# Performance work log

Measured on AMD Instinct MI355X. Metric: run time of the kernel, lower is better.

Reference implementation:

```python
import jax, jax.numpy as jnp
import numpy as np

S, B, H = 1024, 4, 1024
NH, NC = 16, 4            # num_attention_heads, num_combined_heads
HPH = H // NH             # 64
NF = NH // NC             # num_FFN = 4
FFM = 8                   # combined_FFN_multiple
DIN = NC * HPH            # 256, grouped FFN input dim
DHID = FFM * DIN          # 2048, dense_in output dim
DH2 = DHID // 2           # 1024, GLU half / dense_out input dim
EPS = 1e-6
NORM_FACTOR = 1.0 / float(np.sqrt(HPH))


def _ln(x, g, b):
    m = x.mean(-1, keepdims=True)
    v = ((x - m) ** 2).mean(-1, keepdims=True)
    return (x - m) * jax.lax.rsqrt(v + EPS) * g + b


def setup_inputs() -> dict:
    key = jax.random.key(0)
    ks = jax.random.split(key, 10)
    p = lambda k, shape: jax.random.normal(k, shape, jnp.float32) * 0.02
    return {
        "hidden_states": jax.random.normal(ks[0], (S, B, H), jnp.float32),
        "g1": jnp.ones((H,), jnp.float32), "b1": jnp.zeros((H,), jnp.float32),
        "g2": jnp.ones((HPH,), jnp.float32), "b2": jnp.zeros((HPH,), jnp.float32),
        "Wq": p(ks[1], (H, H)), "bq": jnp.zeros((H,), jnp.float32),
        "Wk": p(ks[2], (H, H)), "bk": jnp.zeros((H,), jnp.float32),
        "Wv": p(ks[3], (H, H)), "bv": jnp.zeros((H,), jnp.float32),
        "W_in": p(ks[4], (NF, DIN, DHID)), "b_in": jnp.zeros((NF, DHID), jnp.float32),
        "W_out": p(ks[5], (NF, DH2, DIN)), "b_out": jnp.zeros((NF, DIN), jnp.float32),
        "Wd": p(ks[6], (H, H)), "bd": jnp.zeros((H,), jnp.float32),
    }


def reference(hidden_states, g1, b1, g2, b2, Wq, bq, Wk, bk, Wv, bv,
              W_in, b_in, W_out, b_out, Wd, bd):
    # hidden_states: [S, B, H]
    x = _ln(hidden_states, g1, b1)                       # norm1

    def heads(t):  # [S,B,H] -> [B*NH, S, HPH] (matches view + transpose in torch)
        return jnp.transpose(t.reshape(S, B * NH, HPH), (1, 0, 2))

    q = heads(x @ Wq + bq)
    k = heads(x @ Wk + bk)
    v = heads(x @ Wv + bv)

    # subtraction_gaussian_kernel: pairwise squared euclidean distance
    qk = jnp.einsum('nsd,ntd->nst', q, k)                # [B*NH, S, S]
    q2 = jnp.sum(q * q, axis=-1)
    k2 = jnp.sum(k * k, axis=-1)
    dist = q2[:, :, None] + k2[None if False else slice(None), None, :][0] if False else q2[:, :, None] + k2[:, None, :] - 2.0 * qk
    matmul_result = dist * (-0.5 * NORM_FACTOR)          # scores <= 0

    # Exp sequence op: elementwise exp (softmax replacement, no normalization)
    probs = jnp.exp(matmul_result)

    ctx = jnp.einsum('nst,ntd->nsd', probs, v)           # [B*NH, S, HPH]
    ctx = jnp.transpose(ctx, (1, 0, 2)).reshape(S, B, H)
    ctx = x + ctx                                        # residual with norm1 output (as in source)

    ctx = _ln(ctx.reshape(S, B, NH, HPH), g2, b2)        # per-head norm2

    # grouped FFN over contiguous head subsets (vectorized over the NF groups)
    cg = ctx.reshape(S, B, NF, DIN)
    h = jnp.einsum('sbgi,gio->sbgo', cg, W_in) + b_in    # [S,B,NF,DHID]
    xh, yh = jnp.split(h, 2, axis=-1)
    h = xh * jax.nn.relu(yh)                             # GLU-style x * relu(y)
    og = jnp.einsum('sbgi,gio->sbgo', h, W_out) + b_out  # [S,B,NF,DIN]

    out = og.reshape(S, B, H) @ Wd + bd                  # attention_dense
    return out, matmul_result
```

## Files before the change

kernel.cpp:

```cpp
#include <hip/hip_runtime.h>


typedef __attribute__((ext_vector_type(8))) short short8;
typedef __attribute__((ext_vector_type(4))) float f32x4;

__device__ __forceinline__ unsigned short f2bf(float f) {
  union { float f; unsigned u; } x; x.f = f;
  unsigned r = x.u + 0x7FFFu + ((x.u >> 16) & 1u);
  return (unsigned short)(r >> 16);
}
__device__ __forceinline__ float bf2f(unsigned short u) {
  union { float f; unsigned u; } x; x.u = ((unsigned)u) << 16;
  return x.f;
}
__device__ __forceinline__ unsigned cvtpk(float a, float b) {
  unsigned r;
  asm("v_cvt_pk_bf16_f32 %0, %1, %2" : "=v"(r) : "v"(a), "v"(b));
  return r;
}
__device__ __forceinline__ void gload16(const unsigned short* g, unsigned short* l) {
  __builtin_amdgcn_global_load_lds(
      (const __attribute__((address_space(1))) unsigned int*)g,
      (__attribute__((address_space(3))) unsigned int*)l, 16, 0, 0);
}

__device__ __forceinline__ void ln1_body(
    const float* __restrict__ x, const float* __restrict__ g,
    const float* __restrict__ b,
    unsigned short* __restrict__ ybf, int row, int tid)
{
  const long base = (long)row * 1024;
  const int c = tid * 4;
  float4 v = *(const float4*)(x + base + c);
  float s = v.x + v.y + v.z + v.w;
  float ss = v.x*v.x + v.y*v.y + v.z*v.z + v.w*v.w;
  #pragma unroll
  for (int off = 32; off > 0; off >>= 1) {
    s  += __shfl_xor(s, off);
    ss += __shfl_xor(ss, off);
  }
  __shared__ float sw[4], ssw[4];
  const int wave = tid >> 6;
  if ((tid & 63) == 0) { sw[wave] = s; ssw[wave] = ss; }
  __syncthreads();
  s  = sw[0] + sw[1] + sw[2] + sw[3];
  ss = ssw[0] + ssw[1] + ssw[2] + ssw[3];
  const float mean = s * (1.0f/1024.0f);
  const float var  = ss * (1.0f/1024.0f) - mean*mean;
  const float rs   = rsqrtf(var + 1e-6f);
  const float4 gv = *(const float4*)(g + c);
  const float4 bv = *(const float4*)(b + c);
  const float o0 = (v.x - mean) * rs * gv.x + bv.x;
  const float o1 = (v.y - mean) * rs * gv.y + bv.y;
  const float o2 = (v.z - mean) * rs * gv.z + bv.z;
  const float o3 = (v.w - mean) * rs * gv.w + bv.w;
  uint2 pk; pk.x = cvtpk(o0, o1); pk.y = cvtpk(o2, o3);
  *(uint2*)(ybf + base + c) = pk;
}

__device__ __forceinline__ void transpose_body(
    const float* __restrict__ Wg, unsigned short* __restrict__ WTg,
    int K, int N, int bx, int by, int tid)
{
  __shared__ float T[32][33];
  const int n0 = bx * 32, k0 = by * 32;
  const int r = tid >> 3, c4 = (tid & 7) * 4;
  float4 v = *(const float4*)(Wg + (long)(k0 + r) * N + n0 + c4);
  T[r][c4+0] = v.x; T[r][c4+1] = v.y; T[r][c4+2] = v.z; T[r][c4+3] = v.w;
  __syncthreads();
  ushort4 o;
  o.x = f2bf(T[c4+0][r]); o.y = f2bf(T[c4+1][r]);
  o.z = f2bf(T[c4+2][r]); o.w = f2bf(T[c4+3][r]);
  *(ushort4*)(WTg + (long)(n0 + r) * K + k0 + c4) = o;
}

__global__ __launch_bounds__(256) void prep_all_kernel(
    const float* __restrict__ hs, const float* __restrict__ g1,
    const float* __restrict__ b1,
    unsigned short* __restrict__ xbf,
    const float* __restrict__ Wq, const float* __restrict__ Wk,
    const float* __restrict__ Wv, const float* __restrict__ Wd,
    const float* __restrict__ Win, const float* __restrict__ Wout,
    const float* __restrict__ bq, const float* __restrict__ bk,
    const float* __restrict__ bv,
    unsigned short* __restrict__ wqkvT, unsigned short* __restrict__ wdT,
    unsigned short* __restrict__ winT, unsigned short* __restrict__ woutT,
    float* __restrict__ qkvb)
{
  const int bid = blockIdx.x;
  const int tid = threadIdx.x;
  if (bid < 4096) {
    ln1_body(hs, g1, b1, xbf, bid, tid);
  } else if (bid < 8192) {
    const int idx = bid - 4096;
    const int z = idx >> 10, rem = idx & 1023;
    const float* W = (z == 0) ? Wq : (z == 1) ? Wk : (z == 2) ? Wv : Wd;
    unsigned short* WT = (z == 3) ? wdT : wqkvT + (long)z * 1048576;
    transpose_body(W, WT, 1024, 1024, rem & 31, rem >> 5, tid);
  } else if (bid < 10240) {
    const int rem = bid - 8192;
    const int z = rem >> 9, r2 = rem & 511;
    transpose_body(Win + (long)z * 524288, winT + (long)z * 524288,
                   256, 2048, r2 & 63, r2 >> 6, tid);
  } else if (bid < 11264) {
    const int rem = bid - 10240;
    const int z = rem >> 8, r2 = rem & 255;
    transpose_body(Wout + (long)z * 262144, woutT + (long)z * 262144,
                   1024, 256, r2 & 7, r2 >> 3, tid);
  } else {
    const int i = (bid - 11264) * 256 + tid;
    qkvb[i] = (i < 1024) ? bq[i] : ((i < 2048) ? bk[i - 1024] : bv[i - 2048]);
  }
}

__global__ __launch_bounds__(256) void mfma_gemm_kernel(
    const unsigned short* __restrict__ A, int lda, long agoff,
    const unsigned short* __restrict__ BT, long bgoff, int K,
    const float* __restrict__ bias, int biasoff,
    unsigned short* __restrict__ Cbf, float* __restrict__ Cf,
    int ldc, int cgoff,
    float* __restrict__ q2g, float* __restrict__ k2g)
{
  const int g = blockIdx.z;
  const unsigned short* Ag = A + (long)g * agoff;
  const unsigned short* Bg = BT + (long)g * bgoff;
  const float* biasg = bias + (long)g * biasoff;
  const int row0 = blockIdx.y * 128, col0 = blockIdx.x * 128;
  __shared__ __align__(16) unsigned short As[2][128 * 64];
  __shared__ __align__(16) unsigned short Bs[2][128 * 64];
  const int tid = threadIdx.x;
  const int w = tid >> 6, l = tid & 63;
  const int ms = (w & 1) << 6, ns = (w >> 1) << 6;
  const int fr = l & 15, fg = l >> 4;
  const int lr8 = l >> 3, ls8 = l & 7;
  const int scol = (ls8 ^ lr8) << 3;
  const int rsw = fr & 7;
  f32x4 acc[4][4];
  #pragma unroll
  for (int i = 0; i < 4; ++i)
    #pragma unroll
    for (int j = 0; j < 4; ++j) acc[i][j] = (f32x4)0.0f;

  const int nt = K >> 6;
  #pragma unroll
  for (int sidx = 0; sidx < 2; ++sidx) {
    const int k0 = sidx << 6;
    #pragma unroll
    for (int g8 = 0; g8 < 4; ++g8) {
      const int r = (w << 5) + (g8 << 3);
      gload16(Ag + (long)(row0 + r + lr8) * lda + k0 + scol, &As[sidx][r * 64]);
      gload16(Bg + (long)(col0 + r + lr8) * K  + k0 + scol, &Bs[sidx][r * 64]);
    }
  }
  int cur = 0;
  for (int t = 0; t < nt; ++t) {
    if (t + 1 < nt) asm volatile("s_waitcnt vmcnt(8)" ::: "memory");
    else            asm volatile("s_waitcnt vmcnt(0)" ::: "memory");
    __builtin_amdgcn_s_barrier();
    __builtin_amdgcn_sched_barrier(0);
    short8 af[2][4], bfr[2][4];
    #pragma unroll
    for (int ks = 0; ks < 2; ++ks) {
      const int rslot = (((ks << 2) + fg) ^ rsw) << 3;
      #pragma unroll
      for (int i = 0; i < 4; ++i) {
        af[ks][i]  = *(const short8*)&As[cur][(ms + i*16 + fr) * 64 + rslot];
        bfr[ks][i] = *(const short8*)&Bs[cur][(ns + i*16 + fr) * 64 + rslot];
      }
    }
    asm volatile("s_waitcnt lgkmcnt(0)" ::: "memory");
    __builtin_amdgcn_sched_barrier(0);
    __builtin_amdgcn_s_barrier();
    if (t + 2 < nt) {
      const int k0 = (t + 2) << 6;
      #pragma unroll
      for (int g8 = 0; g8 < 4; ++g8) {
        const int r = (w << 5) + (g8 << 3);
        gload16(Ag + (long)(row0 + r + lr8) * lda + k0 + scol, &As[cur][r * 64]);
        gload16(Bg + (long)(col0 + r + lr8) * K  + k0 + scol, &Bs[cur][r * 64]);
      }
    }
    __builtin_amdgcn_s_setprio(1);
    #pragma unroll
    for (int ks = 0; ks < 2; ++ks)
      #pragma unroll
      for (int i = 0; i < 4; ++i)
        #pragma unroll
        for (int j = 0; j < 4; ++j)
          acc[i][j] = __builtin_amdgcn_mfma_f32_16x16x32_bf16(bfr[ks][j], af[ks][i], acc[i][j], 0, 0, 0);
    __builtin_amdgcn_s_setprio(0);
    cur ^= 1;
  }

  float s2[4] = {0.f, 0.f, 0.f, 0.f};
  #pragma unroll
  for (int j = 0; j < 4; ++j) {
    const float4 bj4 = *(const float4*)(biasg + col0 + ns + j*16 + (fg << 2));
    #pragma unroll
    for (int i = 0; i < 4; ++i) {
      const long row = row0 + ms + i*16 + fr;
      const long cb = row * ldc + (long)g * cgoff + col0 + ns + j*16 + (fg << 2);
      const float v0 = acc[i][j][0] + bj4.x, v1 = acc[i][j][1] + bj4.y;
      const float v2 = acc[i][j][2] + bj4.z, v3 = acc[i][j][3] + bj4.w;
      s2[i] += v0*v0 + v1*v1 + v2*v2 + v3*v3;
      if (Cbf) {
        uint2 pk; pk.x = cvtpk(v0, v1); pk.y = cvtpk(v2, v3);
        *(uint2*)(Cbf + cb) = pk;
      } else {
        f32x4 o = {v0, v1, v2, v3};
        __builtin_nontemporal_store(o, (f32x4*)(Cf + cb));
      }
    }
  }
  if (q2g && col0 < 2048) {
    const int nsAbs = col0 + ns;
    const bool isQ = nsAbs < 1024;
    float* outp = isQ ? q2g : k2g;
    const int head = (isQ ? nsAbs : nsAbs - 1024) >> 6;
    #pragma unroll
    for (int i = 0; i < 4; ++i) {
      float s = s2[i];
      s += __shfl_xor(s, 16);
      s += __shfl_xor(s, 32);
      if (fg == 0) {
        const int gr = row0 + ms + i*16 + fr;
        outp[((gr & 3) * 16 + head) * 1024 + (gr >> 2)] = s;
      }
    }
  }
}

__global__ __launch_bounds__(256) void mfma_gemm64_kernel(
    const unsigned short* __restrict__ A, int lda, long agoff,
    const unsigned short* __restrict__ BT, long bgoff, int K,
    const float* __restrict__ bias, int biasoff,
    unsigned short* __restrict__ Cbf, float* __restrict__ Cf,
    int ldc, int cgoff)
{
  const int g = blockIdx.z;
  const unsigned short* Ag = A + (long)g * agoff;
  const unsigned short* Bg = BT + (long)g * bgoff;
  const float* biasg = bias + (long)g * biasoff;
  const int row0 = blockIdx.y * 128, col0 = blockIdx.x * 64;
  __shared__ __align__(16) unsigned short As[2][128 * 64];
  __shared__ __align__(16) unsigned short Bs[2][64 * 64];
  const int tid = threadIdx.x;
  const int w = tid >> 6, l = tid & 63;
  const int ms = (w & 1) << 6, ns = (w >> 1) << 5;
  const int fr = l & 15, fg = l >> 4;
  const int lr8 = l >> 3, ls8 = l & 7;
  const int scol = (ls8 ^ lr8) << 3;
  const int rsw = fr & 7;
  f32x4 acc[4][2];
  #pragma unroll
  for (int i = 0; i < 4; ++i)
    #pragma unroll
    for (int j = 0; j < 2; ++j) acc[i][j] = (f32x4)0.0f;

  const int nt = K >> 6;
  #pragma unroll
  for (int sidx = 0; sidx < 2; ++sidx) {
    const int k0 = sidx << 6;
    #pragma unroll
    for (int g8 = 0; g8 < 4; ++g8) {
      const int r = (w << 5) + (g8 << 3);
      gload16(Ag + (long)(row0 + r + lr8) * lda + k0 + scol, &As[sidx][r * 64]);
    }
    #pragma unroll
    for (int g8 = 0; g8 < 2; ++g8) {
      const int r = (w << 4) + (g8 << 3);
      gload16(Bg + (long)(col0 + r + lr8) * K + k0 + scol, &Bs[sidx][r * 64]);
    }
  }
  int cur = 0;
  for (int t = 0; t < nt; ++t) {
    if (t + 1 < nt) asm volatile("s_waitcnt vmcnt(6)" ::: "memory");
    else            asm volatile("s_waitcnt vmcnt(0)" ::: "memory");
    __builtin_amdgcn_s_barrier();
    __builtin_amdgcn_sched_barrier(0);
    short8 af[2][4], bfr[2][2];
    #pragma unroll
    for (int ks = 0; ks < 2; ++ks) {
      const int rslot = (((ks << 2) + fg) ^ rsw) << 3;
      #pragma unroll
      for (int i = 0; i < 4; ++i)
        af[ks][i] = *(const short8*)&As[cur][(ms + i*16 + fr) * 64 + rslot];
      #pragma unroll
      for (int j = 0; j < 2; ++j)
        bfr[ks][j] = *(const short8*)&Bs[cur][(ns + j*16 + fr) * 64 + rslot];
    }
    asm volatile("s_waitcnt lgkmcnt(0)" ::: "memory");
    __builtin_amdgcn_sched_barrier(0);
    __builtin_amdgcn_s_barrier();
    if (t + 2 < nt) {
      const int k0 = (t + 2) << 6;
      #pragma unroll
      for (int g8 = 0; g8 < 4; ++g8) {
        const int r = (w << 5) + (g8 << 3);
        gload16(Ag + (long)(row0 + r + lr8) * lda + k0 + scol, &As[cur][r * 64]);
      }
      #pragma unroll
      for (int g8 = 0; g8 < 2; ++g8) {
        const int r = (w << 4) + (g8 << 3);
        gload16(Bg + (long)(col0 + r + lr8) * K + k0 + scol, &Bs[cur][r * 64]);
      }
    }
    __builtin_amdgcn_s_setprio(1);
    #pragma unroll
    for (int ks = 0; ks < 2; ++ks)
      #pragma unroll
      for (int i = 0; i < 4; ++i)
        #pragma unroll
        for (int j = 0; j < 2; ++j)
          acc[i][j] = __builtin_amdgcn_mfma_f32_16x16x32_bf16(bfr[ks][j], af[ks][i], acc[i][j], 0, 0, 0);
    __builtin_amdgcn_s_setprio(0);
    cur ^= 1;
  }

  #pragma unroll
  for (int j = 0; j < 2; ++j) {
    const float4 bj4 = *(const float4*)(biasg + col0 + ns + j*16 + (fg << 2));
    #pragma unroll
    for (int i = 0; i < 4; ++i) {
      const long row = row0 + ms + i*16 + fr;
      const long cb = row * ldc + (long)g * cgoff + col0 + ns + j*16 + (fg << 2);
      const float v0 = acc[i][j][0] + bj4.x, v1 = acc[i][j][1] + bj4.y;
      const float v2 = acc[i][j][2] + bj4.z, v3 = acc[i][j][3] + bj4.w;
      if (Cbf) {
        uint2 pk; pk.x = cvtpk(v0, v1); pk.y = cvtpk(v2, v3);
        *(uint2*)(Cbf + cb) = pk;
      } else {
        f32x4 o = {v0, v1, v2, v3};
        __builtin_nontemporal_store(o, (f32x4*)(Cf + cb));
      }
    }
  }
}

__global__ __launch_bounds__(256) void mfma_glu_kernel(
    const unsigned short* __restrict__ A,
    const unsigned short* __restrict__ WT,
    const float* __restrict__ bin,
    unsigned short* __restrict__ H2)
{
  const int g = blockIdx.z;
  const unsigned short* Ag = A + g * 256;
  const unsigned short* Wg = WT + (long)g * 2048 * 256;
  const float* bg = bin + g * 2048;
  const int row0 = blockIdx.y * 128, col0 = blockIdx.x * 64;
  __shared__ __align__(16) unsigned short As[2][128 * 64];
  __shared__ __align__(16) unsigned short Bxs[2][64 * 64];
  __shared__ __align__(16) unsigned short Bys[2][64 * 64];
  const int tid = threadIdx.x;
  const int w = tid >> 6, l = tid & 63;
  const int ms = (w & 1) << 6, ns = (w >> 1) << 5;
  const int fr = l & 15, fg = l >> 4;
  const int lr8 = l >> 3, ls8 = l & 7;
  const int scol = (ls8 ^ lr8) << 3;
  const int rsw = fr & 7;
  f32x4 ax[4][2], ay[4][2];
  #pragma unroll
  for (int i = 0; i < 4; ++i)
    #pragma unroll
    for (int j = 0; j < 2; ++j) { ax[i][j] = (f32x4)0.0f; ay[i][j] = (f32x4)0.0f; }

  #pragma unroll
  for (int sidx = 0; sidx < 2; ++sidx) {
    const int k0 = sidx << 6;
    #pragma unroll
    for (int g8 = 0; g8 < 4; ++g8) {
      const int r = (w << 5) + (g8 << 3);
      gload16(Ag + (long)(row0 + r + lr8) * 1024 + k0 + scol, &As[sidx][r * 64]);
    }
    #pragma unroll
    for (int g8 = 0; g8 < 2; ++g8) {
      const int r = (w << 4) + (g8 << 3);
      gload16(Wg + (long)(col0 + r + lr8) * 256 + k0 + scol,        &Bxs[sidx][r * 64]);
      gload16(Wg + (long)(1024 + col0 + r + lr8) * 256 + k0 + scol, &Bys[sidx][r * 64]);
    }
  }
  int cur = 0;
  for (int t = 0; t < 4; ++t) {
    if (t + 1 < 4) asm volatile("s_waitcnt vmcnt(8)" ::: "memory");
    else           asm volatile("s_waitcnt vmcnt(0)" ::: "memory");
    __builtin_amdgcn_s_barrier();
    __builtin_amdgcn_sched_barrier(0);
    short8 af[2][4], bx[2][2], by[2][2];
    #pragma unroll
    for (int ks = 0; ks < 2; ++ks) {
      const int rslot = (((ks << 2) + fg) ^ rsw) << 3;
      #pragma unroll
      for (int i = 0; i < 4; ++i)
        af[ks][i] = *(const short8*)&As[cur][(ms + i*16 + fr) * 64 + rslot];
      #pragma unroll
      for (int j = 0; j < 2; ++j) {
        bx[ks][j] = *(const short8*)&Bxs[cur][(ns + j*16 + fr) * 64 + rslot];
        by[ks][j] = *(const short8*)&Bys[cur][(ns + j*16 + fr) * 64 + rslot];
      }
    }
    asm volatile("s_waitcnt lgkmcnt(0)" ::: "memory");
    __builtin_amdgcn_sched_barrier(0);
    __builtin_amdgcn_s_barrier();
    if (t + 2 < 4) {
      const int k0 = (t + 2) << 6;
      #pragma unroll
      for (int g8 = 0; g8 < 4; ++g8) {
        const int r = (w << 5) + (g8 << 3);
        gload16(Ag + (long)(row0 + r + lr8) * 1024 + k0 + scol, &As[cur][r * 64]);
      }
      #pragma unroll
      for (int g8 = 0; g8 < 2; ++g8) {
        const int r = (w << 4) + (g8 << 3);
        gload16(Wg + (long)(col0 + r + lr8) * 256 + k0 + scol,        &Bxs[cur][r * 64]);
        gload16(Wg + (long)(1024 + col0 + r + lr8) * 256 + k0 + scol, &Bys[cur][r * 64]);
      }
    }
    __builtin_amdgcn_s_setprio(1);
    #pragma unroll
    for (int ks = 0; ks < 2; ++ks)
      #pragma unroll
      for (int i = 0; i < 4; ++i)
        #pragma unroll
        for (int j = 0; j < 2; ++j) {
          ax[i][j] = __builtin_amdgcn_mfma_f32_16x16x32_bf16(bx[ks][j], af[ks][i], ax[i][j], 0, 0, 0);
          ay[i][j] = __builtin_amdgcn_mfma_f32_16x16x32_bf16(by[ks][j], af[ks][i], ay[i][j], 0, 0, 0);
        }
    __builtin_amdgcn_s_setprio(0);
    cur ^= 1;
  }

  #pragma unroll
  for (int j = 0; j < 2; ++j) {
    const float4 bx4 = *(const float4*)(bg + col0 + ns + j*16 + (fg << 2));
    const float4 by4 = *(const float4*)(bg + 1024 + col0 + ns + j*16 + (fg << 2));
    #pragma unroll
    for (int i = 0; i < 4; ++i) {
      const long row = row0 + ms + i*16 + fr;
      const long cb = row * 4096 + g * 1024 + col0 + ns + j*16 + (fg << 2);
      float o4[4];
      const float* bxp = &bx4.x; const float* byp = &by4.x;
      #pragma unroll
      for (int r4 = 0; r4 < 4; ++r4) {
        const float xh = ax[i][j][r4] + bxp[r4];
        const float yh = ay[i][j][r4] + byp[r4];
        o4[r4] = xh * fmaxf(yh, 0.0f);
      }
      uint2 pk; pk.x = cvtpk(o4[0], o4[1]); pk.y = cvtpk(o4[2], o4[3]);
      *(uint2*)(H2 + cb) = pk;
    }
  }
}

__global__ __launch_bounds__(256) void vtrans_kernel(
    const unsigned short* __restrict__ qkv, unsigned short* __restrict__ vt)
{
  __shared__ unsigned short T[64][72];
  const int n = blockIdx.y, s0 = blockIdx.x * 64;
  const int b = n >> 4, hoff = (n & 15) * 64;
  const int tid = threadIdx.x;
  #pragma unroll
  for (int p = 0; p < 2; ++p) {
    const int r = (tid >> 3) + p * 32, c = (tid & 7) << 3;
    *(short8*)&T[r][c] = *(const short8*)(qkv + ((long)((s0 + r) * 4 + b)) * 3072 + 2048 + hoff + c);
  }
  __syncthreads();
  #pragma unroll
  for (int p = 0; p < 2; ++p) {
    const int d = (tid >> 3) + p * 32, sc = (tid & 7) << 3;
    short8 o;
    #pragma unroll
    for (int j = 0; j < 8; ++j) o[j] = (short)T[sc + j][d];
    *(short8*)(vt + ((long)n * 64 + d) * 1024 + s0 + sc) = o;
  }
}

__global__ __launch_bounds__(256) void attn_kernel(
    const unsigned short* __restrict__ qkv, const unsigned short* __restrict__ vt,
    const float* __restrict__ q2g, const float* __restrict__ k2g,
    const unsigned short* __restrict__ xbf, const float* __restrict__ g2,
    const float* __restrict__ b2,
    unsigned short* __restrict__ ctx2, float* __restrict__ scores)
{
  const int n = blockIdx.y;
  const int s0 = blockIdx.x * 64;
  const int b = n >> 4, hoff = (n & 15) * 64;
  __shared__ __align__(16) unsigned short Qs[64 * 64];
  __shared__ __align__(16) unsigned short Ks[2][64 * 64];
  __shared__ __align__(16) unsigned short VTl[2][64 * 64];
  __shared__ __align__(16) unsigned short Ps[64 * 64];
  __shared__ float k2s[1024];
  const int tid = threadIdx.x, w = tid >> 6, l = tid & 63;
  const int fr = l & 15, fg = l >> 4;
  const int lr8 = l >> 3, ls8 = l & 7;
  const int sslot = ((ls8 ^ lr8) << 3);
  const int rsw = fr & 7;

  #pragma unroll
  for (int p = 0; p < 2; ++p) {
    const int r = (tid >> 3) + p * 32, cs = tid & 7;
    *(short8*)&Qs[r * 64 + ((cs ^ (r & 7)) << 3)] =
        *(const short8*)(qkv + ((long)((s0 + r) * 4 + b)) * 3072 + hoff + (cs << 3));
  }
  *(float4*)&k2s[tid << 2] = *(const float4*)(k2g + n * 1024 + (tid << 2));
  float q2m[4];
  #pragma unroll
  for (int i = 0; i < 4; ++i) q2m[i] = -0.0625f * q2g[n * 1024 + s0 + i*16 + fr];
  #pragma unroll
  for (int p = 0; p < 2; ++p) {
    const int rowb = p * 32 + w * 8;
    gload16(qkv + ((long)((rowb + lr8) * 4 + b)) * 3072 + 1024 + hoff + sslot, &Ks[0][rowb * 64]);
    gload16(vt + ((long)n * 64 + rowb + lr8) * 1024 + sslot,                   &VTl[0][rowb * 64]);
  }
  __syncthreads();

  f32x4 o[4];
  #pragma unroll
  for (int i = 0; i < 4; ++i) o[i] = (f32x4)0.0f;

  int cur = 0;
  for (int t0 = 0; t0 < 1024; t0 += 64) {
    if (t0 > 0) {
      asm volatile("s_waitcnt vmcnt(4)" ::: "memory");
      __builtin_amdgcn_sched_barrier(0);
      __builtin_amdgcn_s_barrier();
    }
    f32x4 c4[4];
    #pragma unroll
    for (int i = 0; i < 4; ++i) c4[i] = (f32x4)0.0f;
    #pragma unroll
    for (int ks = 0; ks < 2; ++ks) {
      const short8 kf = *(const short8*)&Ks[cur][((w << 4) + fr) * 64 + ((((ks << 2) + fg) ^ rsw) << 3)];
      #pragma unroll
      for (int i = 0; i < 4; ++i) {
        const short8 qf = *(const short8*)&Qs[(i*16 + fr) * 64 + ((((ks << 2) + fg) ^ rsw) << 3)];
        c4[i] = __builtin_amdgcn_mfma_f32_16x16x32_bf16(kf, qf, c4[i], 0, 0, 0);
      }
    }
    if (t0 + 64 < 1024) {
      #pragma unroll
      for (int p = 0; p < 2; ++p) {
        const int rowb = p * 32 + w * 8;
        gload16(qkv + ((long)((t0 + 64 + rowb + lr8) * 4 + b)) * 3072 + 1024 + hoff + sslot,
                &Ks[cur ^ 1][rowb * 64]);
        gload16(vt + ((long)n * 64 + rowb + lr8) * 1024 + t0 + 64 + sslot,
                &VTl[cur ^ 1][rowb * 64]);
      }
    }
    const float4 k2v4 = *(const float4*)&k2s[t0 + (w << 4) + (fg << 2)];
    const float k2m[4] = {-0.0625f*k2v4.x, -0.0625f*k2v4.y, -0.0625f*k2v4.z, -0.0625f*k2v4.w};
    #pragma unroll
    for (int i = 0; i < 4; ++i) {
      f32x4 sc;
      float pe[4];
      #pragma unroll
      for (int r4 = 0; r4 < 4; ++r4) {
        const float m = fmaf(c4[i][r4], 0.125f, q2m[i] + k2m[r4]);
        sc[r4] = m;
        pe[r4] = __expf(m);
      }
      __builtin_nontemporal_store(sc,
          (f32x4*)(scores + (long)n * 1048576 + (long)(s0 + i*16 + fr) * 1024 + t0 + (w << 4) + (fg << 2)));
      const int slot = (w << 1) + (fg >> 1);
      const int pc = ((slot ^ (fr & 7)) << 3) + ((fg & 1) << 2);
      uint2 pk; pk.x = cvtpk(pe[0], pe[1]); pk.y = cvtpk(pe[2], pe[3]);
      *(uint2*)&Ps[(i*16 + fr) * 64 + pc] = pk;
    }
    asm volatile("s_waitcnt lgkmcnt(0)" ::: "memory");
    __builtin_amdgcn_sched_barrier(0);
    __builtin_amdgcn_s_barrier();
    #pragma unroll
    for (int ks = 0; ks < 2; ++ks) {
      const short8 vb = *(const short8*)&VTl[cur][((w << 4) + fr) * 64 + ((((ks << 2) + fg) ^ rsw) << 3)];
      #pragma unroll
      for (int i = 0; i < 4; ++i) {
        const short8 pf = *(const short8*)&Ps[(i*16 + fr) * 64 + ((((ks << 2) + fg) ^ rsw) << 3)];
        o[i] = __builtin_amdgcn_mfma_f32_16x16x32_bf16(vb, pf, o[i], 0, 0, 0);
      }
    }
    asm volatile("s_waitcnt lgkmcnt(0)" ::: "memory");
    __builtin_amdgcn_sched_barrier(0);
    __builtin_amdgcn_s_barrier();
    cur ^= 1;
  }

  const int dbase = (w << 4) + (fg << 2);
  float xf[4][4];
  #pragma unroll
  for (int i = 0; i < 4; ++i) {
    const ushort4 xu = *(const ushort4*)(xbf + ((long)((s0 + i*16 + fr) * 4 + b)) * 1024 + hoff + dbase);
    xf[i][0] = bf2f(xu.x); xf[i][1] = bf2f(xu.y);
    xf[i][2] = bf2f(xu.z); xf[i][3] = bf2f(xu.w);
  }

  float* redbuf = (float*)&Ps[0];
  const int slot = (w << 2) + fg;
  #pragma unroll
  for (int i = 0; i < 4; ++i) {
    float s = 0.f, ss = 0.f;
    #pragma unroll
    for (int r4 = 0; r4 < 4; ++r4) {
      const float v = o[i][r4] + xf[i][r4];
      s += v; ss = fmaf(v, v, ss);
    }
    redbuf[(i*16 + fr) * 16 + slot] = s;
    redbuf[1024 + (i*16 + fr) * 16 + slot] = ss;
  }
  __syncthreads();
  float* statbuf = (float*)&Qs[0];
  {
    const int row = tid >> 2, q4 = tid & 3;
    float s = 0.f, ss = 0.f;
    #pragma unroll
    for (int k = 0; k < 4; ++k) {
      s  += redbuf[row * 16 + q4 * 4 + k];
      ss += redbuf[1024 + row * 16 + q4 * 4 + k];
    }
    s  += __shfl_xor(s, 1);  s  += __shfl_xor(s, 2);
    ss += __shfl_xor(ss, 1); ss += __shfl_xor(ss, 2);
    if (q4 == 0) {
      const float mean = s * (1.0f/64.0f);
      const float var  = ss * (1.0f/64.0f) - mean * mean;
      statbuf[row] = mean;
      statbuf[64 + row] = rsqrtf(var + 1e-6f);
    }
  }
  __syncthreads();
  const float4 g2v = *(const float4*)(g2 + dbase);
  const float4 b2v = *(const float4*)(b2 + dbase);
  const float* gp = &g2v.x; const float* bp = &b2v.x;
  #pragma unroll
  for (int i = 0; i < 4; ++i) {
    const float mean = statbuf[i*16 + fr];
    const float rs   = statbuf[64 + i*16 + fr];
    float vo[4];
    #pragma unroll
    for (int r4 = 0; r4 < 4; ++r4)
      vo[r4] = (o[i][r4] + xf[i][r4] - mean) * rs * gp[r4] + bp[r4];
    uint2 pk; pk.x = cvtpk(vo[0], vo[1]); pk.y = cvtpk(vo[2], vo[3]);
    *(uint2*)(ctx2 + ((long)((s0 + i*16 + fr) * 4 + b)) * 1024 + hoff + dbase) = pk;
  }
}

extern "C" void kernel_launch(void* const* d_in, const int* in_sizes, int n_in,
                              void* d_out, int out_size, void* d_ws, size_t ws_size,
                              hipStream_t stream) {
  const float* hs   = (const float*)d_in[0];
  const float* g1   = (const float*)d_in[1];
  const float* b1   = (const float*)d_in[2];
  const float* g2   = (const float*)d_in[3];
  const float* b2   = (const float*)d_in[4];
  const float* Wq   = (const float*)d_in[5];
  const float* bq   = (const float*)d_in[6];
  const float* Wk   = (const float*)d_in[7];
  const float* bk   = (const float*)d_in[8];
  const float* Wv   = (const float*)d_in[9];
  const float* bv   = (const float*)d_in[10];
  const float* Win  = (const float*)d_in[11];
  const float* bin  = (const float*)d_in[12];
  const float* Wout = (const float*)d_in[13];
  const float* bout = (const float*)d_in[14];
  const float* Wd   = (const float*)d_in[15];
  const float* bd   = (const float*)d_in[16];

  char* ws = (char*)d_ws;
  unsigned short* qkv   = (unsigned short*)(ws + 0);
  unsigned short* xbf   = (unsigned short*)(ws + 25165824);
  unsigned short* ctx2  = (unsigned short*)(ws + 33554432);
  unsigned short* vt    = (unsigned short*)(ws + 41943040);
  unsigned short* wqkvT = (unsigned short*)(ws + 50331648);
  unsigned short* winT  = (unsigned short*)(ws + 56623104);
  unsigned short* woutT = (unsigned short*)(ws + 60817408);
  unsigned short* wdT   = (unsigned short*)(ws + 62914560);
  float*          qkvb  = (float*)(ws + 65011712);
  float*          q2g   = (float*)(ws + 65024000);
  float*          k2g   = (float*)(ws + 65286144);
  unsigned short* h2    = (unsigned short*)(ws + 0);
  unsigned short* og    = (unsigned short*)(ws + 41943040);

  float* out0 = (float*)d_out;
  float* out1 = out0 + 4194304;

  prep_all_kernel<<<11276, 256, 0, stream>>>(
      hs, g1, b1, xbf,
      Wq, Wk, Wv, Wd, Win, Wout, bq, bk, bv,
      wqkvT, wdT, winT, woutT, qkvb);

  mfma_gemm_kernel<<<dim3(24,32,1), 256, 0, stream>>>(
      xbf, 1024, 0, wqkvT, 0, 1024, qkvb, 0, qkv, nullptr, 3072, 0, q2g, k2g);

  vtrans_kernel<<<dim3(16,64), 256, 0, stream>>>(qkv, vt);

  attn_kernel<<<dim3(16,64), 256, 0, stream>>>(qkv, vt, q2g, k2g, xbf, g2, b2, ctx2, out1);

  mfma_glu_kernel<<<dim3(16,32,4), 256, 0, stream>>>(ctx2, winT, bin, h2);

  mfma_gemm64_kernel<<<dim3(4,32,4), 256, 0, stream>>>(
      h2, 4096, 1024, woutT, 262144, 1024, bout, 256, og, nullptr, 1024, 256);

  mfma_gemm64_kernel<<<dim3(16,32,1), 256, 0, stream>>>(
      og, 1024, 0, wdT, 0, 1024, bd, 0, nullptr, out0, 1024, 0);
}
```

Baseline: 225.0 us.

## Replace QKV GEMM with 256x256-tile 512-thread kernel and split-k interleaved LDS reads

The generic 128x128 GEMM for the QKV projection is replaced by a specialized kernel that computes 256x256 tiles with 8 waves, each wave owning a 128x64 sub-tile. Staging in LDS is doubled, to 64KB per buffer pair. The inner loop now issues the first k-half's MFMAs before reading the second k-half's fragments, overlapping LDS reads with compute. The larger tiles raise arithmetic intensity and cut global reloads, but the grid shrinks to 192 blocks, which may underfill the 256 CUs, and register pressure from 32 accumulators rises.

```diff
diff --git a/kernel.cpp b/kernel.cpp
--- a/kernel.cpp
+++ b/kernel.cpp
@@ -113,112 +113,117 @@
   }
 }
 
-__global__ __launch_bounds__(256) void mfma_gemm_kernel(
-    const unsigned short* __restrict__ A, int lda, long agoff,
-    const unsigned short* __restrict__ BT, long bgoff, int K,
-    const float* __restrict__ bias, int biasoff,
-    unsigned short* __restrict__ Cbf, float* __restrict__ Cf,
-    int ldc, int cgoff,
+__global__ __launch_bounds__(512) void qkv256_kernel(
+    const unsigned short* __restrict__ A,
+    const unsigned short* __restrict__ BT,
+    const float* __restrict__ bias,
+    unsigned short* __restrict__ C,
     float* __restrict__ q2g, float* __restrict__ k2g)
 {
-  const int g = blockIdx.z;
-  const unsigned short* Ag = A + (long)g * agoff;
-  const unsigned short* Bg = BT + (long)g * bgoff;
-  const float* biasg = bias + (long)g * biasoff;
-  const int row0 = blockIdx.y * 128, col0 = blockIdx.x * 128;
-  __shared__ __align__(16) unsigned short As[2][128 * 64];
-  __shared__ __align__(16) unsigned short Bs[2][128 * 64];
+  const int row0 = blockIdx.y * 256, col0 = blockIdx.x * 256;
+  __shared__ __align__(16) unsigned short As[2][256 * 64];
+  __shared__ __align__(16) unsigned short Bs[2][256 * 64];
   const int tid = threadIdx.x;
   const int w = tid >> 6, l = tid & 63;
-  const int ms = (w & 1) << 6, ns = (w >> 1) << 6;
+  const int ms = (w >> 2) << 7;
+  const int ns = (w & 3) << 6;
   const int fr = l & 15, fg = l >> 4;
   const int lr8 = l >> 3, ls8 = l & 7;
   const int scol = (ls8 ^ lr8) << 3;
   const int rsw = fr & 7;
-  f32x4 acc[4][4];
-  #pragma unroll
-  for (int i = 0; i < 4; ++i)
+  f32x4 acc[8][4];
+  #pragma unroll
+  for (int i = 0; i < 8; ++i)
     #pragma unroll
     for (int j = 0; j < 4; ++j) acc[i][j] = (f32x4)0.0f;
 
-  const int nt = K >> 6;
   #pragma unroll
   for (int sidx = 0; sidx < 2; ++sidx) {
     const int k0 = sidx << 6;
     #pragma unroll
     for (int g8 = 0; g8 < 4; ++g8) {
-      const int r = (w << 5) + (g8 << 3);
-      gload16(Ag + (long)(row0 + r + lr8) * lda + k0 + scol, &As[sidx][r * 64]);
-      gload16(Bg + (long)(col0 + r + lr8) * K  + k0 + scol, &Bs[sidx][r * 64]);
+      const int rb = (g8 << 6) + (w << 3);
+      gload16(A  + (long)(row0 + rb + lr8) * 1024 + k0 + scol, &As[sidx][rb * 64]);
+      gload16(BT + (long)(col0 + rb + lr8) * 1024 + k0 + scol, &Bs[sidx][rb * 64]);
     }
   }
   int cur = 0;
-  for (int t = 0; t < nt; ++t) {
-    if (t + 1 < nt) asm volatile("s_waitcnt vmcnt(8)" ::: "memory");
-    else            asm volatile("s_waitcnt vmcnt(0)" ::: "memory");
+  for (int t = 0; t < 16; ++t) {
+    if (t < 15) asm volatile("s_waitcnt vmcnt(8)" ::: "memory");
+    else        asm volatile("s_waitcnt vmcnt(0)" ::: "memory");
     __builtin_amdgcn_s_barrier();
     __builtin_amdgcn_sched_barrier(0);
-    short8 af[2][4], bfr[2][4];
-    #pragma unroll
-    for (int ks = 0; ks < 2; ++ks) {
-      const int rslot = (((ks << 2) + fg) ^ rsw) << 3;
-      #pragma unroll
-      for (int i = 0; i < 4; ++i) {
-        af[ks][i]  = *(const short8*)&As[cur][(ms + i*16 + fr) * 64 + rslot];
-        bfr[ks][i] = *(const short8*)&Bs[cur][(ns + i*16 + fr) * 64 + rslot];
-      }
+    {
+      const int rslot = (fg ^ rsw) << 3;
+      short8 af[8], b4[4];
+      #pragma unroll
+      for (int i = 0; i < 8; ++i)
+        af[i] = *(const short8*)&As[cur][(ms + i*16 + fr) * 64 + rslot];
+      #pragma unroll
+      for (int j = 0; j < 4; ++j)
+        b4[j] = *(const short8*)&Bs[cur][(ns + j*16 + fr) * 64 + rslot];
+      #pragma unroll
+      for (int i = 0; i < 8; ++i)
+        #pragma unroll
+        for (int j = 0; j < 4; ++j)
+          acc[i][j] = __builtin_amdgcn_mfma_f32_16x16x32_bf16(b4[j], af[i], acc[i][j], 0, 0, 0);
+    }
+    short8 af1[8], b41[4];
+    {
+      const int rslot = ((4 + fg) ^ rsw) << 3;
+      #pragma unroll
+      for (int i = 0; i < 8; ++i)
+        af1[i] = *(const short8*)&As[cur][(ms + i*16 + fr) * 64 + rslot];
+      #pragma unroll
+      for (int j = 0; j < 4; ++j)
+        b41[j] = *(const short8*)&Bs[cur][(ns + j*16 + fr) * 64 + rslot];
     }
     asm volatile("s_waitcnt lgkmcnt(0)" ::: "memory");
     __builtin_amdgcn_sched_barrier(0);
     __builtin_amdgcn_s_barrier();
-    if (t + 2 < nt) {
+    if (t + 2 < 16) {
       const int k0 = (t + 2) << 6;
       #pragma unroll
       for (int g8 = 0; g8 < 4; ++g8) {
-        const int r = (w << 5) + (g8 << 3);
-        gload16(Ag + (long)(row0 + r + lr8) * lda + k0 + scol, &As[cur][r * 64]);
-        gload16(Bg + (long)(col0 + r + lr8) * K  + k0 + scol, &Bs[cur][r * 64]);
+        const int rb = (g8 << 6) + (w << 3);
+        gload16(A  + (long)(row0 + rb + lr8) * 1024 + k0 + scol, &As[cur][rb * 64]);
+        gload16(BT + (long)(col0 + rb + lr8) * 1024 + k0 + scol, &Bs[cur][rb * 64]);
       }
     }
     __builtin_amdgcn_s_setprio(1);
     #pragma unroll
-    for (int ks = 0; ks < 2; ++ks)
-      #pragma unroll
-      for (int i = 0; i < 4; ++i)
-        #pragma unroll
-        for (int j = 0; j < 4; ++j)
-          acc[i][j] = __builtin_amdgcn_mfma_f32_16x16x32_bf16(bfr[ks][j], af[ks][i], acc[i][j], 0, 0, 0);
+    for (int i = 0; i < 8; ++i)
+      #pragma unroll
+      for (int j = 0; j < 4; ++j)
+        acc[i][j] = __builtin_amdgcn_mfma_f32_16x16x32_bf16(b41[j], af1[i], acc[i][j], 0, 0, 0);
     __builtin_amdgcn_s_setprio(0);
     cur ^= 1;
   }
 
-  float s2[4] = {0.f, 0.f, 0.f, 0.f};
+  float s2[8];
+  #pragma unroll
+  for (int i = 0; i < 8; ++i) s2[i] = 0.f;
   #pragma unroll
   for (int j = 0; j < 4; ++j) {
-    const float4 bj4 = *(const float4*)(biasg + col0 + ns + j*16 + (fg << 2));
-    #pragma unroll
-    for (int i = 0; i < 4; ++i) {
+    const float4 bj4 = *(const float4*)(bias + col0 + ns + j*16 + (fg << 2));
+    #pragma unroll
+    for (int i = 0; i < 8; ++i) {
       const long row = row0 + ms + i*16 + fr;
-      const long cb = row * ldc + (long)g * cgoff + col0 + ns + j*16 + (fg << 2);
+      const long cb = row * 3072 + col0 + ns + j*16 + (fg << 2);
       const float v0 = acc[i][j][0] + bj4.x, v1 = acc[i][j][1] + bj4.y;
       const float v2 = acc[i][j][2] + bj4.z, v3 = acc[i][j][3] + bj4.w;
       s2[i] += v0*v0 + v1*v1 + v2*v2 + v3*v3;
-      if (Cbf) {
-        uint2 pk; pk.x = cvtpk(v0, v1); pk.y = cvtpk(v2, v3);
-        *(uint2*)(Cbf + cb) = pk;
-      } else {
-        f32x4 o = {v0, v1, v2, v3};
-        __builtin_nontemporal_store(o, (f32x4*)(Cf + cb));
-      }
-    }
-  }
-  if (q2g && col0 < 2048) {
-    const int nsAbs = col0 + ns;
+      uint2 pk; pk.x = cvtpk(v0, v1); pk.y = cvtpk(v2, v3);
+      *(uint2*)(C + cb) = pk;
+    }
+  }
+  const int nsAbs = col0 + ns;
+  if (nsAbs < 2048) {
     const bool isQ = nsAbs < 1024;
     float* outp = isQ ? q2g : k2g;
     const int head = (isQ ? nsAbs : nsAbs - 1024) >> 6;
     #pragma unroll
-    for (int i = 0; i < 4; ++i) {
+    for (int i = 0; i < 8; ++i) {
       float s = s2[i];
       s += __shfl_xor(s, 16);
       s += __shfl_xor(s, 32);
@@ -685,8 +690,8 @@
       Wq, Wk, Wv, Wd, Win, Wout, bq, bk, bv,
       wqkvT, wdT, winT, woutT, qkvb);
 
-  mfma_gemm_kernel<<<dim3(24,32,1), 256, 0, stream>>>(
-      xbf, 1024, 0, wqkvT, 0, 1024, qkvb, 0, qkv, nullptr, 3072, 0, q2g, k2g);
+  qkv256_kernel<<<dim3(12,16,1), 512, 0, stream>>>(
+      xbf, wqkvT, qkvb, qkv, q2g, k2g);
 
   vtrans_kernel<<<dim3(16,64), 256, 0, stream>>>(qkv, vt);
 
```

Measured after the change: 224.5 us. No clear change (-0.2%).
